# Kernel tuning notes

Hardware: AMD Instinct MI355X
Metric: run time of the kernel (lower is better)

The kernel has to match this reference:

```python
import jax, jax.numpy as jnp
import numpy as np

N_OPCODES = 31
B, S, D = 64, 16, 1024
MAX_STEPS = 16


def setup_inputs() -> dict:
    key = jax.random.key(0)
    k1, k2, k3, k4 = jax.random.split(key, 4)
    return {
        "opcode_logits": jax.random.normal(k1, (B, S, N_OPCODES), dtype=jnp.float32),
        "operands": jax.random.normal(k2, (B, S, 4), dtype=jnp.float32),
        "signal": jax.random.normal(k3, (B, D), dtype=jnp.float32),
        "op_kernels": jax.random.normal(k4, (N_OPCODES, D, D), dtype=jnp.float32) * 0.01,
    }


def reference(opcode_logits, operands, signal, op_kernels):
    # opcode_logits: (B,S,O), operands: (B,S,4), signal: (B,D), op_kernels: (O,D,D)
    n_steps = min(opcode_logits.shape[1], MAX_STEPS)
    weights = jax.nn.softmax(opcode_logits, axis=-1)  # (B,S,O)

    # time-major inputs for scan: (n_steps, B, O) and (n_steps, B, 1)
    ws = jnp.swapaxes(weights[:, :n_steps], 0, 1)
    gate_logits = jnp.swapaxes(operands[:, :n_steps, 3:4], 0, 1)

    def step(h, inputs):
        w, gl = inputs  # (B,O), (B,1)
        gate = jax.nn.sigmoid(gl)
        # equivalent to h @ (sum_o w_o K_o) but never forms the (B,D,D) kernel
        transformed = jnp.einsum('bo,bd,odk->bk', w, h, op_kernels)
        h_new = gate * transformed + (1.0 - gate) * h
        return h_new, None

    h, _ = jax.lax.scan(step, signal, (ws, gate_logits))
    return h
```

## Files before the change

### kernel.cpp

```cpp
#include <hip/hip_runtime.h>
#include <cstddef>
#include <cstdint>

#define NB 64
#define ND 1024
#define NO 31
#define NSTEPS 16
#define KS 124
#define KT32 992
#define KC32 8

typedef _Float16 half8 __attribute__((ext_vector_type(8)));
typedef float floatx4 __attribute__((ext_vector_type(4)));

__global__ void softmax_k(const float* __restrict__ logits, float* __restrict__ W) {
    int row = blockIdx.x * blockDim.x + threadIdx.x;
    if (row >= NB * NSTEPS) return;
    const float* x = logits + (size_t)row * NO;
    float m = -1e30f;
    for (int o = 0; o < NO; ++o) m = fmaxf(m, x[o]);
    float e[NO]; float s = 0.f;
    for (int o = 0; o < NO; ++o) { e[o] = expf(x[o] - m); s += e[o]; }
    float inv = 1.0f / s;
    float* wo = W + (size_t)row * NO;
    for (int o = 0; o < NO; ++o) wo[o] = e[o] * inv;
}

__global__ __launch_bounds__(256) void kconv_k(const float* __restrict__ K,
                                               _Float16* __restrict__ Ktf) {
    __shared__ float tile[32 * 256];
    int kt  = blockIdx.x >> 2;
    int nb4 = blockIdx.x & 3;
    int tid = threadIdx.x;
    int lane = tid & 63, w = tid >> 6;

    {
        const float* src = K + ((size_t)kt * 32) * ND + nb4 * 256;
        #pragma unroll
        for (int i = 0; i < 8; ++i) {
            int r = i * 4 + w;
            int x = lane * 4;
            int xs = x ^ (((r >> 3) & 1) << 4);
            float4 v = *(const float4*)(src + (size_t)r * ND + x);
            *(float4*)&tile[r * 256 + xs] = v;
        }
    }
    __syncthreads();

    int kl0 = (lane >> 4) * 8;
    int swz = ((lane >> 4) & 1) << 4;
    #pragma unroll
    for (int i = 0; i < 4; ++i) {
        int ns_local = i * 4 + w;
        int nl = ns_local * 16 + (lane & 15);
        int xsw = nl ^ swz;
        half8 v;
        #pragma unroll
        for (int j = 0; j < 8; ++j) v[j] = (_Float16)tile[(kl0 + j) * 256 + xsw];
        int ns = nb4 * 16 + ns_local;
        size_t unit = ((size_t)ns * KT32 + kt) * 64 + lane;
        *(half8*)(Ktf + unit * 8) = v;
    }
}

__global__ __launch_bounds__(256) void gemm_k(
    const float* __restrict__ h, const _Float16* __restrict__ Ktf,
    const float* __restrict__ W, float* __restrict__ P, int step)
{
    __shared__ _Float16 lds_a[64 * 256];
    int nb = blockIdx.x;
    int ks = blockIdx.y;
    int tid = threadIdx.x;
    int l = tid & 63, w = tid >> 6;
    int o = ks >> 2;
    int d_base = (ks & 3) * 256;

    {
        int b = tid >> 2, u = tid & 3;
        float wv = W[((size_t)b * NSTEPS + step) * NO + o];
        const float* hb = h + (size_t)b * ND + d_base;
        #pragma unroll
        for (int li = 0; li < 8; ++li) {
            int p = li * 4 + u;
            float4 x0 = *(const float4*)(hb + p * 8);
            float4 x1 = *(const float4*)(hb + p * 8 + 4);
            half8 v;
            v[0] = (_Float16)(x0.x * wv); v[1] = (_Float16)(x0.y * wv);
            v[2] = (_Float16)(x0.z * wv); v[3] = (_Float16)(x0.w * wv);
            v[4] = (_Float16)(x1.x * wv); v[5] = (_Float16)(x1.y * wv);
            v[6] = (_Float16)(x1.z * wv); v[7] = (_Float16)(x1.w * wv);
            *(half8*)&lds_a[(size_t)(p * 64 + b) * 8] = v;
        }
    }
    __syncthreads();

    int ml = l & 15, q = l >> 4;
    int ns0 = nb * 16 + w * 4;
    const half8* Ap = (const half8*)lds_a;

    half8 breg[4][8];
    #pragma unroll
    for (int t = 0; t < 4; ++t) {
        const half8* bp = (const half8*)Ktf
            + ((size_t)(ns0 + t) * KT32 + (size_t)ks * KC32) * 64 + l;
        #pragma unroll
        for (int s = 0; s < 8; ++s) breg[t][s] = bp[(size_t)s * 64];
    }

    floatx4 acc[4][4] = {};
    #pragma unroll
    for (int s = 0; s < 8; ++s) {
        int abase = (s * 4 + q) * 64 + ml;
        half8 a0 = Ap[abase];
        half8 a1 = Ap[abase + 16];
        half8 a2 = Ap[abase + 32];
        half8 a3 = Ap[abase + 48];
        #pragma unroll
        for (int t = 0; t < 4; ++t) {
            acc[t][0] = __builtin_amdgcn_mfma_f32_16x16x32_f16(a0, breg[t][s], acc[t][0], 0, 0, 0);
            acc[t][1] = __builtin_amdgcn_mfma_f32_16x16x32_f16(a1, breg[t][s], acc[t][1], 0, 0, 0);
            acc[t][2] = __builtin_amdgcn_mfma_f32_16x16x32_f16(a2, breg[t][s], acc[t][2], 0, 0, 0);
            acc[t][3] = __builtin_amdgcn_mfma_f32_16x16x32_f16(a3, breg[t][s], acc[t][3], 0, 0, 0);
        }
    }

    float* Pks = P + (size_t)ks * (NB * ND);
    #pragma unroll
    for (int t = 0; t < 4; ++t) {
        int n = (ns0 + t) * 16 + ml;
        #pragma unroll
        for (int mt = 0; mt < 4; ++mt) {
            #pragma unroll
            for (int r = 0; r < 4; ++r) {
                int b = mt * 16 + q * 4 + r;
                Pks[(size_t)b * ND + n] = acc[t][mt][r];
            }
        }
    }
}

__global__ void update_k(const float* __restrict__ hin, const float* __restrict__ P,
                         const float* __restrict__ operands, float* __restrict__ hout,
                         int step)
{
    __shared__ float red[256];
    int tid = threadIdx.x;
    int w = tid >> 6, o = tid & 63;
    int gbase = blockIdx.x * 64;
    int g = gbase + o;
    const float* p = P + (size_t)(w * 31) * (NB * ND) + g;
    float s = 0.f;
    #pragma unroll
    for (int i = 0; i < 31; ++i) s += p[(size_t)i * (NB * ND)];
    red[tid] = s;
    __syncthreads();
    if (tid < 64) {
        float tot = red[tid] + red[tid + 64] + red[tid + 128] + red[tid + 192];
        int b = g >> 10;
        float gl = operands[((size_t)b * NSTEPS + step) * 4 + 3];
        float gt = 1.0f / (1.0f + expf(-gl));
        hout[g] = gt * tot + (1.0f - gt) * hin[g];
    }
}

extern "C" void kernel_launch(void* const* d_in, const int* in_sizes, int n_in,
                              void* d_out, int out_size, void* d_ws, size_t ws_size,
                              hipStream_t stream)
{
    const float* logits   = (const float*)d_in[0];
    const float* operands = (const float*)d_in[1];
    const float* signal   = (const float*)d_in[2];
    const float* opk      = (const float*)d_in[3];
    float* out = (float*)d_out;
    char* ws = (char*)d_ws;

    size_t offW = 0;
    size_t offP = 131072;
    size_t offH = offP + (size_t)KS * NB * ND * 4;
    size_t offK = offH + 2ull * NB * ND * 4;

    float*    W  = (float*)(ws + offW);
    float*    P  = (float*)(ws + offP);
    float*    h0 = (float*)(ws + offH);
    float*    h1 = h0 + NB * ND;
    _Float16* Ktf = (_Float16*)(ws + offK);

    softmax_k<<<dim3(4), 256, 0, stream>>>(logits, W);
    kconv_k<<<dim3(3968), 256, 0, stream>>>(opk, Ktf);

    const float* hc = signal;
    float* hn = h0;
    for (int t = 0; t < NSTEPS; ++t) {
        gemm_k<<<dim3(4, KS), 256, 0, stream>>>(hc, Ktf, W, P, t);
        float* dst = (t == NSTEPS - 1) ? out : hn;
        update_k<<<dim3(1024), 256, 0, stream>>>(hc, P, operands, dst, t);
        hc = dst;
        hn = (hn == h0) ? h1 : h0;
    }
}
```

Measured before the change: 586.0 us.

## Halve split-K partials by intra-block K reduction in GEMM

```diff
diff --git a/kernel.cpp b/kernel.cpp
--- a/kernel.cpp
+++ b/kernel.cpp
@@ -6,9 +6,9 @@
 #define ND 1024
 #define NO 31
 #define NSTEPS 16
-#define KS 124
+#define KS 62
 #define KT32 992
-#define KC32 8
+#define KC32 16
 
 typedef _Float16 half8 __attribute__((ext_vector_type(8)));
 typedef float floatx4 __attribute__((ext_vector_type(4)));
@@ -63,25 +63,25 @@
     }
 }
 
-__global__ __launch_bounds__(256) void gemm_k(
+__global__ __launch_bounds__(512) void gemm_k(
     const float* __restrict__ h, const _Float16* __restrict__ Ktf,
     const float* __restrict__ W, float* __restrict__ P, int step)
 {
-    __shared__ _Float16 lds_a[64 * 256];
+    __shared__ _Float16 lds_a[64 * 512];
     int nb = blockIdx.x;
     int ks = blockIdx.y;
     int tid = threadIdx.x;
     int l = tid & 63, w = tid >> 6;
-    int o = ks >> 2;
-    int d_base = (ks & 3) * 256;
+    int o = ks >> 1;
+    int d_base = (ks & 1) * 512;
 
     {
-        int b = tid >> 2, u = tid & 3;
+        int b = tid >> 3, u = tid & 7;
         float wv = W[((size_t)b * NSTEPS + step) * NO + o];
         const float* hb = h + (size_t)b * ND + d_base;
         #pragma unroll
         for (int li = 0; li < 8; ++li) {
-            int p = li * 4 + u;
+            int p = li * 8 + u;
             float4 x0 = *(const float4*)(hb + p * 8);
             float4 x1 = *(const float4*)(hb + p * 8 + 4);
             half8 v;
@@ -95,14 +95,15 @@
     __syncthreads();
 
     int ml = l & 15, q = l >> 4;
-    int ns0 = nb * 16 + w * 4;
+    int wn = w & 3, kh = w >> 2;
+    int ns0 = nb * 16 + wn * 4;
     const half8* Ap = (const half8*)lds_a;
 
     half8 breg[4][8];
     #pragma unroll
     for (int t = 0; t < 4; ++t) {
         const half8* bp = (const half8*)Ktf
-            + ((size_t)(ns0 + t) * KT32 + (size_t)ks * KC32) * 64 + l;
+            + ((size_t)(ns0 + t) * KT32 + (size_t)(ks * KC32 + kh * 8)) * 64 + l;
         #pragma unroll
         for (int s = 0; s < 8; ++s) breg[t][s] = bp[(size_t)s * 64];
     }
@@ -110,7 +111,7 @@
     floatx4 acc[4][4] = {};
     #pragma unroll
     for (int s = 0; s < 8; ++s) {
-        int abase = (s * 4 + q) * 64 + ml;
+        int abase = ((kh * 8 + s) * 4 + q) * 64 + ml;
         half8 a0 = Ap[abase];
         half8 a1 = Ap[abase + 16];
         half8 a2 = Ap[abase + 32];
@@ -124,16 +125,29 @@
         }
     }
 
-    float* Pks = P + (size_t)ks * (NB * ND);
-    #pragma unroll
-    for (int t = 0; t < 4; ++t) {
-        int n = (ns0 + t) * 16 + ml;
-        #pragma unroll
-        for (int mt = 0; mt < 4; ++mt) {
+    __syncthreads();
+    floatx4* lred = (floatx4*)lds_a;
+    if (kh == 1) {
+        #pragma unroll
+        for (int t = 0; t < 4; ++t)
             #pragma unroll
-            for (int r = 0; r < 4; ++r) {
-                int b = mt * 16 + q * 4 + r;
-                Pks[(size_t)b * ND + n] = acc[t][mt][r];
+            for (int mt = 0; mt < 4; ++mt)
+                lred[(t * 4 + mt) * 256 + wn * 64 + l] = acc[t][mt];
+    }
+    __syncthreads();
+    if (kh == 0) {
+        float* Pks = P + (size_t)ks * (NB * ND);
+        #pragma unroll
+        for (int t = 0; t < 4; ++t) {
+            int n = (ns0 + t) * 16 + ml;
+            #pragma unroll
+            for (int mt = 0; mt < 4; ++mt) {
+                floatx4 other = lred[(t * 4 + mt) * 256 + wn * 64 + l];
+                #pragma unroll
+                for (int r = 0; r < 4; ++r) {
+                    int b = mt * 16 + q * 4 + r;
+                    Pks[(size_t)b * ND + n] = acc[t][mt][r] + other[r];
+                }
             }
         }
     }
@@ -145,21 +159,22 @@
 {
     __shared__ float red[256];
     int tid = threadIdx.x;
-    int w = tid >> 6, o = tid & 63;
-    int gbase = blockIdx.x * 64;
-    int g = gbase + o;
-    const float* p = P + (size_t)(w * 31) * (NB * ND) + g;
+    int w = tid >> 6, lane = tid & 63;
+    int j = (w & 1) * 64 + lane;
+    int g = blockIdx.x * 128 + j;
+    const float* p = P + (size_t)((w >> 1) * 31) * (NB * ND) + g;
     float s = 0.f;
     #pragma unroll
     for (int i = 0; i < 31; ++i) s += p[(size_t)i * (NB * ND)];
-    red[tid] = s;
-    __syncthreads();
-    if (tid < 64) {
-        float tot = red[tid] + red[tid + 64] + red[tid + 128] + red[tid + 192];
-        int b = g >> 10;
+    red[(w >> 1) * 128 + j] = s;
+    __syncthreads();
+    if (tid < 128) {
+        float tot = red[tid] + red[tid + 128];
+        int g2 = blockIdx.x * 128 + tid;
+        int b = g2 >> 10;
         float gl = operands[((size_t)b * NSTEPS + step) * 4 + 3];
         float gt = 1.0f / (1.0f + expf(-gl));
-        hout[g] = gt * tot + (1.0f - gt) * hin[g];
+        hout[g2] = gt * tot + (1.0f - gt) * hin[g2];
     }
 }
 
@@ -191,9 +206,9 @@
     const float* hc = signal;
     float* hn = h0;
     for (int t = 0; t < NSTEPS; ++t) {
-        gemm_k<<<dim3(4, KS), 256, 0, stream>>>(hc, Ktf, W, P, t);
+        gemm_k<<<dim3(4, KS), 512, 0, stream>>>(hc, Ktf, W, P, t);
         float* dst = (t == NSTEPS - 1) ? out : hn;
-        update_k<<<dim3(1024), 256, 0, stream>>>(hc, P, operands, dst, t);
+        update_k<<<dim3(512), 256, 0, stream>>>(hc, P, operands, dst, t);
         hc = dst;
         hn = (hn == h0) ? h1 : h0;
     }
```

After: 524.6 us. 1.12x faster.
